# Kernel tuning notes

Measured on AMD Instinct MI355X. Metric: run time of the kernel, lower is better.

## Reference

```python
import jax, jax.numpy as jnp
import numpy as np

CH = 256
HEADS = 4
RED = 8  # SE reduction on 2*CH channels


def _conv2d(x, w, pad):
    # x: [b,c,h,w], w: [o,i,kh,kw]
    return jax.lax.conv_general_dilated(
        x, w, window_strides=(1, 1), padding=[(pad, pad), (pad, pad)],
        dimension_numbers=('NCHW', 'OIHW', 'NCHW'))


def setup_inputs() -> dict:
    key = jax.random.key(0)
    ks = jax.random.split(key, 12)
    b, c, h, w = 4, CH, 64, 64
    c2 = 2 * c
    s = 0.02
    inp = {
        'color_feat': jax.random.normal(ks[0], (b, c, h, w), jnp.float32),
        'gray_feat': jax.random.normal(ks[1], (b, c, h, w), jnp.float32),
        'Wq': jax.random.normal(ks[2], (c, c), jnp.float32) * s,
        'Wk': jax.random.normal(ks[3], (c, c), jnp.float32) * s,
        'Wv': jax.random.normal(ks[4], (c, c), jnp.float32) * s,
        'Wproj': jax.random.normal(ks[5], (c, c), jnp.float32) * s,
        'ca_w1': jax.random.normal(ks[6], (c2 // RED, c2), jnp.float32) * s,
        'ca_w2': jax.random.normal(ks[7], (c2, c2 // RED), jnp.float32) * s,
        'sa_w': jax.random.normal(ks[8], (1, 2, 7, 7), jnp.float32) * s,
        'fuse_w': jax.random.normal(ks[9], (c, c2, 3, 3), jnp.float32) * s,
        'bn_gamma': jnp.ones((c,), jnp.float32),
        'bn_beta': jnp.zeros((c,), jnp.float32),
        'bn_mean': jnp.zeros((c,), jnp.float32),
        'bn_var': jnp.ones((c,), jnp.float32),
    }
    return inp


def reference(color_feat, gray_feat, Wq, Wk, Wv, Wproj, ca_w1, ca_w2,
              sa_w, fuse_w, bn_gamma, bn_beta, bn_mean, bn_var):
    b, c, h, w = color_feat.shape
    nh = HEADS
    d = c // nh
    scale = d ** -0.5

    def heads(x, W):
        # 1x1 conv then split heads: [b,c,h,w] -> [b,nh,hw,d]
        y = jnp.einsum('bchw,oc->bohw', x, W)
        return y.reshape(b, nh, d, h * w).transpose(0, 1, 3, 2)

    q = heads(color_feat, Wq)
    k = heads(gray_feat, Wk)
    v = heads(gray_feat, Wv)

    attn = jax.nn.softmax(jnp.einsum('bnid,bnjd->bnij', q, k) * scale, axis=-1)
    out = jnp.einsum('bnij,bnjd->bnid', attn, v)
    out = out.transpose(0, 1, 3, 2).reshape(b, c, h, w)
    out = jnp.einsum('bchw,oc->bohw', out, Wproj)

    cat = jnp.concatenate([out, gray_feat], axis=1)  # [b,2c,h,w]

    # Channel attention (SE with shared MLP on avg- and max-pooled vectors)
    def mlp(z):
        return jax.nn.relu(z @ ca_w1.T) @ ca_w2.T
    avg = cat.mean(axis=(2, 3))
    mx = cat.max(axis=(2, 3))
    wch = jax.nn.sigmoid(mlp(avg) + mlp(mx))[:, :, None, None]
    cat = cat * wch

    # Spatial attention: channel-mean/max -> 7x7 conv -> sigmoid gate
    sa_in = jnp.stack([cat.mean(axis=1), cat.max(axis=1)], axis=1)  # [b,2,h,w]
    wsp = jax.nn.sigmoid(_conv2d(sa_in, sa_w, pad=3))
    cat = cat * wsp

    # Fuse: 3x3 conv -> BatchNorm (inference stats) -> LeakyReLU(0.2)
    y = _conv2d(cat, fuse_w, pad=1)
    inv = bn_gamma / jnp.sqrt(bn_var + 1e-5)
    y = (y - bn_mean[None, :, None, None]) * inv[None, :, None, None] + bn_beta[None, :, None, None]
    return jnp.where(y > 0, y, 0.2 * y)
```

## Files before the change

### kernel.cpp

```cpp
#include <hip/hip_runtime.h>
#include <hip/hip_bf16.h>
#include <stdint.h>

#define HW_ 4096

typedef short bf16x8 __attribute__((ext_vector_type(8)));
typedef short short4v __attribute__((ext_vector_type(4)));
typedef short short8v __attribute__((ext_vector_type(8)));
typedef float f32x4 __attribute__((ext_vector_type(4)));
typedef float f32x16 __attribute__((ext_vector_type(16)));
typedef uint32_t u32x4 __attribute__((ext_vector_type(4)));

__device__ inline unsigned short f2bf(float x) {
  uint32_t u = __builtin_bit_cast(uint32_t, x);
  uint32_t r = ((u >> 16) & 1u) + 0x7fffu;
  return (unsigned short)((u + r) >> 16);
}
__device__ inline uint32_t cvt_pk_bf16(float lo, float hi) {
  uint32_t r;
  asm("v_cvt_pk_bf16_f32 %0, %1, %2" : "=v"(r) : "v"(lo), "v"(hi));
  return r;
}
__device__ inline float bf_lo(uint32_t u) { return __builtin_bit_cast(float, u << 16); }
__device__ inline float bf_hi(uint32_t u) { return __builtin_bit_cast(float, u & 0xffff0000u); }
__device__ inline void gld_lds16(const unsigned short* g, unsigned short* l) {
  __builtin_amdgcn_global_load_lds((const __attribute__((address_space(1))) void*)g,
                                   (__attribute__((address_space(3))) void*)l, 16, 0, 0);
}

#define WAIT_BARRIER(VMSTR)                                                  \
  asm volatile("s_waitcnt " VMSTR "\n\ts_barrier" ::: "memory");             \
  __builtin_amdgcn_sched_barrier(0);

__global__ __launch_bounds__(256) void xconv_kernel(
    const float* __restrict__ X, unsigned short* __restrict__ Y) {
  const int i = blockIdx.x * 256 + threadIdx.x;
  const int p = i & 4095;
  const int cg = (i >> 12) & 31;
  const int b = i >> 17;
  const float* src = X + ((size_t)b * 256 + cg * 8) * HW_ + p;
  float v[8];
#pragma unroll
  for (int e = 0; e < 8; ++e) v[e] = src[(size_t)e * HW_];
  uint4 o;
  o.x = cvt_pk_bf16(v[0], v[1]);
  o.y = cvt_pk_bf16(v[2], v[3]);
  o.z = cvt_pk_bf16(v[4], v[5]);
  o.w = cvt_pk_bf16(v[6], v[7]);
  *(uint4*)&Y[((size_t)(b * 32 + cg) * HW_ + p) * 8] = o;
}

__global__ __launch_bounds__(256) void prep_kernel(
    const float* __restrict__ Wq, const float* __restrict__ Wk,
    const float* __restrict__ Wv, const float* __restrict__ Wp,
    const float* __restrict__ fw,
    unsigned short* __restrict__ WqB, unsigned short* __restrict__ WkB,
    unsigned short* __restrict__ WvB, unsigned short* __restrict__ WpB,
    unsigned short* __restrict__ wt) {
  const int blk = blockIdx.x;
  if (blk < 128) {
    const int which = blk >> 5;
    const float* W = which == 0 ? Wq : which == 1 ? Wk : which == 2 ? Wv : Wp;
    unsigned short* Y = which == 0 ? WqB : which == 1 ? WkB : which == 2 ? WvB : WpB;
    const int i = (blk & 31) * 256 + threadIdx.x;
    const int o = i & 255;
    const int cg = i >> 8;
    float4 a = *(const float4*)&W[(size_t)o * 256 + cg * 8];
    float4 bq = *(const float4*)&W[(size_t)o * 256 + cg * 8 + 4];
    uint4 ov;
    ov.x = cvt_pk_bf16(a.x, a.y);
    ov.y = cvt_pk_bf16(a.z, a.w);
    ov.z = cvt_pk_bf16(bq.x, bq.y);
    ov.w = cvt_pk_bf16(bq.z, bq.w);
    *(uint4*)&Y[((size_t)cg * 256 + o) * 8] = ov;
  } else {
    const size_t i = (size_t)(blk - 128) * 256 + threadIdx.x;
    const int oc = (int)(i >> 9);
    const int ic = (int)(i & 511);
    const float* src = fw + i * 9;
#pragma unroll
    for (int tap = 0; tap < 9; ++tap)
      wt[((size_t)tap * 256 + oc) * 512 + ic] = f2bf(src[tap]);
  }
}

#define GSTAGE(KS, BUF)                                                       \
  gld_lds16(Xb + ((size_t)((KS) * 2 + (t >> 7)) * HW_ + p0 + (t & 127)) * 8,  \
            &X_l[BUF][0][0][0] + (size_t)t * 8);
#define GCOMP(KS)                                                             \
  {                                                                           \
    bf16x8 af = *(const bf16x8*)&W_l[(KS) * 2 + g32][wo * 32 + n][0];         \
    bf16x8 b0 = *(const bf16x8*)&X_l[(KS) & 3][g32][wp * 64 + n][0];          \
    bf16x8 b1 = *(const bf16x8*)&X_l[(KS) & 3][g32][wp * 64 + 32 + n][0];     \
    acc[0] = __builtin_amdgcn_mfma_f32_32x32x16_bf16(af, b0, acc[0], 0, 0, 0);\
    acc[1] = __builtin_amdgcn_mfma_f32_32x32x16_bf16(af, b1, acc[1], 0, 0, 0);\
  }

__global__ __launch_bounds__(256) void gemm_mfma_kernel(
    const unsigned short* __restrict__ Xbf, const unsigned short* __restrict__ Wbf,
    void* __restrict__ Yv, int mode, float oscale) {
  __shared__ unsigned short W_l[32][64][8];
  __shared__ unsigned short X_l[4][2][128][8];
  const int t = threadIdx.x;
  const int w = t >> 6;
  const int l = t & 63;
  const int n = l & 31;
  const int g32 = l >> 5;
  const int p0 = blockIdx.x * 128;
  const int o0 = blockIdx.y * 64;
  const int b = blockIdx.z;
  const int wo = w >> 1, wp = w & 1;
  const unsigned short* Xb = Xbf + (size_t)b * 32 * HW_ * 8;

#pragma unroll
  for (int j = 0; j < 8; ++j) {
    const int i = j * 256 + t;
    gld_lds16(Wbf + ((size_t)(i >> 6) * 256 + o0 + (i & 63)) * 8,
              &W_l[0][0][0] + (size_t)i * 8);
  }
  GSTAGE(0, 0)
  GSTAGE(1, 1)
  GSTAGE(2, 2)

  f32x16 acc[2] = {};
  for (int ks = 0; ks < 13; ++ks) {
    WAIT_BARRIER("vmcnt(2)")
    GSTAGE(ks + 3, (ks + 3) & 3)
    GCOMP(ks)
  }
  WAIT_BARRIER("vmcnt(2)")
  GCOMP(13)
  WAIT_BARRIER("vmcnt(1)")
  GCOMP(14)
  WAIT_BARRIER("vmcnt(0)")
  GCOMP(15)

  if (mode == 1) {
    unsigned short* Y = (unsigned short*)Yv;
    const size_t bh = (size_t)b * 4 + blockIdx.y;
#pragma unroll
    for (int pf = 0; pf < 2; ++pf) {
      const int p = p0 + wp * 64 + pf * 32 + n;
      unsigned short* dst = Y + (bh * HW_ + p) * 64 + wo * 32 + 4 * g32;
#pragma unroll
      for (int q = 0; q < 4; ++q) {
        uint2 uu;
        uu.x = cvt_pk_bf16(acc[pf][q * 4 + 0] * oscale, acc[pf][q * 4 + 1] * oscale);
        uu.y = cvt_pk_bf16(acc[pf][q * 4 + 2] * oscale, acc[pf][q * 4 + 3] * oscale);
        *(uint2*)&dst[8 * q] = uu;
      }
    }
  } else if (mode == 2) {
    unsigned short* Y = (unsigned short*)Yv;
#pragma unroll
    for (int pf = 0; pf < 2; ++pf) {
      const int p = p0 + wp * 64 + pf * 32 + n;
#pragma unroll
      for (int r = 0; r < 16; ++r) {
        const int m = (r & 3) + 8 * (r >> 2) + 4 * g32;
        Y[((size_t)b * 256 + o0 + wo * 32 + m) * HW_ + p] = f2bf(acc[pf][r]);
      }
    }
  } else {
    unsigned short* Y = (unsigned short*)Yv;
    const int cgb = (o0 + wo * 32) >> 3;
#pragma unroll
    for (int pf = 0; pf < 2; ++pf) {
      const int p = p0 + wp * 64 + pf * 32 + n;
#pragma unroll
      for (int q = 0; q < 4; ++q) {
        uint2 uu;
        uu.x = cvt_pk_bf16(acc[pf][q * 4 + 0], acc[pf][q * 4 + 1]);
        uu.y = cvt_pk_bf16(acc[pf][q * 4 + 2], acc[pf][q * 4 + 3]);
        *(uint2*)&Y[((size_t)(b * 32 + cgb + q) * HW_ + p) * 8 + 4 * g32] = uu;
      }
    }
  }
}

#define ATTN_STAGE(SB)                                                       \
  {                                                                          \
    gld_lds16(gKp, kst + (SB) * 4096);                                       \
    gld_lds16(gKp + 8 * 64, kst + (SB) * 4096 + 512);                        \
    gld_lds16(gVp, vst + (SB) * 4096);                                       \
    gld_lds16(gVp + (size_t)8 * HW_, vst + (SB) * 4096 + 512);               \
    gKp += 4096;                                                             \
    gVp += 64;                                                               \
  }

#define ATTN_COMPUTE(BUF)                                                    \
  {                                                                          \
    f32x16 aS0 = zero16, aS1 = zero16;                                       \
    _Pragma("unroll") for (int s = 0; s < 4; ++s) {                          \
      bf16x8 kf0 = *(const bf16x8*)&k_l[(BUF) * 4096 + rowKA + kox[s]];      \
      bf16x8 kf1 = *(const bf16x8*)&k_l[(BUF) * 4096 + rowKB + kox[s]];      \
      aS0 = __builtin_amdgcn_mfma_f32_32x32x16_bf16(kf0, qf[s], aS0, 0, 0, 0); \
      aS1 = __builtin_amdgcn_mfma_f32_32x32x16_bf16(kf1, qf[s], aS1, 0, 0, 0); \
    }                                                                        \
    float ex0[16], ex1[16];                                                  \
    float rs = 0.f;                                                          \
    _Pragma("unroll") for (int r = 0; r < 16; ++r) {                         \
      ex0[r] = __builtin_amdgcn_exp2f(aS0[r]);                               \
      ex1[r] = __builtin_amdgcn_exp2f(aS1[r]);                               \
      rs += ex0[r] + ex1[r];                                                 \
    }                                                                        \
    l_r += rs;                                                               \
    union { u32x4 u4; bf16x8 v8; } pA, pB, pC, pD;                           \
    pA.u4 = (u32x4){cvt_pk_bf16(ex0[0], ex0[1]), cvt_pk_bf16(ex0[2], ex0[3]),    \
                    cvt_pk_bf16(ex0[4], ex0[5]), cvt_pk_bf16(ex0[6], ex0[7])};   \
    pB.u4 = (u32x4){cvt_pk_bf16(ex0[8], ex0[9]), cvt_pk_bf16(ex0[10], ex0[11]),  \
                    cvt_pk_bf16(ex0[12], ex0[13]), cvt_pk_bf16(ex0[14], ex0[15])};\
    pC.u4 = (u32x4){cvt_pk_bf16(ex1[0], ex1[1]), cvt_pk_bf16(ex1[2], ex1[3]),    \
                    cvt_pk_bf16(ex1[4], ex1[5]), cvt_pk_bf16(ex1[6], ex1[7])};   \
    pD.u4 = (u32x4){cvt_pk_bf16(ex1[8], ex1[9]), cvt_pk_bf16(ex1[10], ex1[11]),  \
                    cvt_pk_bf16(ex1[12], ex1[13]), cvt_pk_bf16(ex1[14], ex1[15])};\
    _Pragma("unroll") for (int dh = 0; dh < 2; ++dh) {                       \
      const int rw = (BUF) * 4096 + (dh * 32 + n) * 64;                      \
      union { short4v h2[2]; bf16x8 v8; } v0, v1, v2, v3;                    \
      v0.h2[0] = *(const short4v*)&v_l[rw + voA0];                           \
      v0.h2[1] = *(const short4v*)&v_l[rw + voA1];                           \
      v1.h2[0] = *(const short4v*)&v_l[rw + voB0];                           \
      v1.h2[1] = *(const short4v*)&v_l[rw + voB1];                           \
      v2.h2[0] = *(const short4v*)&v_l[rw + voC0];                           \
      v2.h2[1] = *(const short4v*)&v_l[rw + voC1];                           \
      v3.h2[0] = *(const short4v*)&v_l[rw + voD0];                           \
      v3.h2[1] = *(const short4v*)&v_l[rw + voD1];                           \
      f32x16 ac = accO[dh];                                                  \
      ac = __builtin_amdgcn_mfma_f32_32x32x16_bf16(v0.v8, pA.v8, ac, 0, 0, 0); \
      ac = __builtin_amdgcn_mfma_f32_32x32x16_bf16(v1.v8, pB.v8, ac, 0, 0, 0); \
      ac = __builtin_amdgcn_mfma_f32_32x32x16_bf16(v2.v8, pC.v8, ac, 0, 0, 0); \
      ac = __builtin_amdgcn_mfma_f32_32x32x16_bf16(v3.v8, pD.v8, ac, 0, 0, 0); \
      accO[dh] = ac;                                                         \
    }                                                                        \
  }

#define ATTN_PHASE(B, SB, VMSTR, DOST)                                       \
  WAIT_BARRIER(VMSTR)                                                        \
  if (DOST) { ATTN_STAGE(SB) }                                               \
  ATTN_COMPUTE(B)

__global__ __launch_bounds__(256) void attn_mfma_kernel(
    const unsigned short* __restrict__ Qb, const unsigned short* __restrict__ Kb,
    const unsigned short* __restrict__ Vb, unsigned short* __restrict__ Abf) {
  __shared__ unsigned short k_l[4 * 4096];
  __shared__ unsigned short v_l[4 * 4096];
  const int t = threadIdx.x;
  const int w = t >> 6;
  const int l = t & 63;
  const int n = l & 31;
  const int h = l >> 5;
  const int bid = blockIdx.x;
  const int gidx = (bid & 7) * 64 + (bid >> 3);
  const int bn = gidx >> 5;
  const int q0 = (gidx & 31) * 128 + w * 32;

  bf16x8 qf[4];
#pragma unroll
  for (int s = 0; s < 4; ++s)
    qf[s] = *(const bf16x8*)&Qb[((size_t)bn * HW_ + q0 + n) * 64 + s * 16 + h * 8];

  const int n7 = n & 7;
  const int rowKA = n * 64;
  const int rowKB = (32 + n) * 64;
  int kox[4];
#pragma unroll
  for (int s = 0; s < 4; ++s) kox[s] = ((2 * s + h) ^ n7) * 8;
  const int h4 = 4 * h;
  const int voA0 = ((0 ^ n7) * 8) + h4, voA1 = ((1 ^ n7) * 8) + h4;
  const int voB0 = ((2 ^ n7) * 8) + h4, voB1 = ((3 ^ n7) * 8) + h4;
  const int voC0 = ((4 ^ n7) * 8) + h4, voC1 = ((5 ^ n7) * 8) + h4;
  const int voD0 = ((6 ^ n7) * 8) + h4, voD1 = ((7 ^ n7) * 8) + h4;

  const int srow = 16 * w + (l >> 3);
  const int schunk = (l & 7) ^ ((l >> 3) & 7);
  const unsigned short* gKp = Kb + ((size_t)bn * HW_ + srow) * 64 + schunk * 8;
  const unsigned short* gVp = Vb + ((size_t)bn * 64 + srow) * HW_ + schunk * 8;
  unsigned short* kst = k_l + w * 1024;
  unsigned short* vst = v_l + w * 1024;

  f32x16 accO[2] = {};
  float l_r = 0.f;
  const f32x16 zero16 = {};

  ATTN_STAGE(0)
  ATTN_STAGE(1)

  for (int t4 = 0; t4 < 15; ++t4) {
    ATTN_PHASE(0, 2, "vmcnt(4)", 1)
    ATTN_PHASE(1, 3, "vmcnt(4)", 1)
    ATTN_PHASE(2, 0, "vmcnt(4)", 1)
    ATTN_PHASE(3, 1, "vmcnt(4)", 1)
  }
  ATTN_PHASE(0, 2, "vmcnt(4)", 1)
  ATTN_PHASE(1, 3, "vmcnt(4)", 1)
  ATTN_PHASE(2, 0, "vmcnt(4)", 0)
  ATTN_PHASE(3, 0, "vmcnt(0)", 0)

  const int head = bn & 3;
  const int bb = bn >> 2;
  const float lsum = l_r + __shfl_xor(l_r, 32);
  const float inv = 1.0f / lsum;
  const int pcol = q0 + n;
#pragma unroll
  for (int dh = 0; dh < 2; ++dh)
#pragma unroll
    for (int k4 = 0; k4 < 4; ++k4) {
      uint2 uu;
      uu.x = cvt_pk_bf16(accO[dh][k4 * 4 + 0] * inv, accO[dh][k4 * 4 + 1] * inv);
      uu.y = cvt_pk_bf16(accO[dh][k4 * 4 + 2] * inv, accO[dh][k4 * 4 + 3] * inv);
      const int cg = head * 8 + dh * 4 + k4;
      *(uint2*)&Abf[((size_t)(bb * 32 + cg) * HW_ + pcol) * 8 + h4] = uu;
    }
}

__global__ __launch_bounds__(256) void pool_kernel(
    const unsigned short* __restrict__ Pbf, const unsigned short* __restrict__ Gbf,
    float* __restrict__ psum, float* __restrict__ pmaxH) {
  const int cg = blockIdx.x;
  const int b = blockIdx.y;
  const int half = blockIdx.z;
  const int t = threadIdx.x;
  const unsigned short* P = Pbf + ((size_t)(b * 32 + cg) * HW_ + half * 2048) * 8;
  const unsigned short* G = Gbf + ((size_t)(b * 32 + cg) * HW_ + half * 2048) * 8;
  float s[16], m[16];
#pragma unroll
  for (int i = 0; i < 16; ++i) { s[i] = 0.f; m[i] = -1e30f; }
  for (int p = t; p < 2048; p += 256) {
    uint4 a = *(const uint4*)&P[(size_t)p * 8];
    uint4 gg = *(const uint4*)&G[(size_t)p * 8];
    const uint32_t ua[4] = {a.x, a.y, a.z, a.w};
    const uint32_t ug[4] = {gg.x, gg.y, gg.z, gg.w};
#pragma unroll
    for (int q = 0; q < 4; ++q) {
      const float a0 = bf_lo(ua[q]), a1 = bf_hi(ua[q]);
      const float g0 = bf_lo(ug[q]), g1 = bf_hi(ug[q]);
      s[q * 2] += a0; s[q * 2 + 1] += a1;
      m[q * 2] = fmaxf(m[q * 2], a0); m[q * 2 + 1] = fmaxf(m[q * 2 + 1], a1);
      s[8 + q * 2] += g0; s[8 + q * 2 + 1] += g1;
      m[8 + q * 2] = fmaxf(m[8 + q * 2], g0); m[8 + q * 2 + 1] = fmaxf(m[8 + q * 2 + 1], g1);
    }
  }
#pragma unroll
  for (int i = 0; i < 16; ++i)
#pragma unroll
    for (int off = 1; off < 64; off <<= 1) {
      s[i] += __shfl_xor(s[i], off);
      m[i] = fmaxf(m[i], __shfl_xor(m[i], off));
    }
  __shared__ float red[4][32];
  const int wv = t >> 6;
  if ((t & 63) == 0) {
#pragma unroll
    for (int i = 0; i < 16; ++i) { red[wv][i] = s[i]; red[wv][16 + i] = m[i]; }
  }
  __syncthreads();
  if (t < 32) {
    const float v0 = red[0][t], v1 = red[1][t], v2 = red[2][t], v3 = red[3][t];
    if (t < 16) {
      const int ch = (t < 8) ? cg * 8 + t : 256 + cg * 8 + (t - 8);
      psum[half * 2048 + b * 512 + ch] = v0 + v1 + v2 + v3;
    } else {
      const int i = t - 16;
      const int ch = (i < 8) ? cg * 8 + i : 256 + cg * 8 + (i - 8);
      pmaxH[half * 2048 + b * 512 + ch] = fmaxf(fmaxf(v0, v1), fmaxf(v2, v3));
    }
  }
}

__global__ __launch_bounds__(256) void se_kernel(
    const float* __restrict__ psum, const float* __restrict__ pmaxH,
    const float* __restrict__ w1, const float* __restrict__ w2,
    float* __restrict__ wch) {
  const int b = blockIdx.x;
  const int t = threadIdx.x;
  __shared__ float za[512], zm[512], hs[64];
  za[t] = (psum[b * 512 + t] + psum[2048 + b * 512 + t]) * (1.f / 4096.f);
  za[256 + t] = (psum[b * 512 + 256 + t] + psum[2048 + b * 512 + 256 + t]) * (1.f / 4096.f);
  zm[t] = fmaxf(pmaxH[b * 512 + t], pmaxH[2048 + b * 512 + t]);
  zm[256 + t] = fmaxf(pmaxH[b * 512 + 256 + t], pmaxH[2048 + b * 512 + 256 + t]);
  __syncthreads();
  if (t < 64) {
    float ha = 0.f, hm = 0.f;
    for (int c = 0; c < 512; ++c) {
      const float w = w1[t * 512 + c];
      ha += w * za[c];
      hm += w * zm[c];
    }
    hs[t] = fmaxf(ha, 0.f) + fmaxf(hm, 0.f);
  }
  __syncthreads();
  for (int o = t; o < 512; o += 256) {
    float acc = 0.f;
#pragma unroll
    for (int hh = 0; hh < 64; ++hh) acc += hs[hh] * w2[o * 64 + hh];
    wch[b * 512 + o] = 1.f / (1.f + __expf(-acc));
  }
}

__global__ __launch_bounds__(256) void sa_reduce_kernel(
    const unsigned short* __restrict__ Pbf, const unsigned short* __restrict__ Gbf,
    const float* __restrict__ wch, float* __restrict__ sa_in) {
  const int b = blockIdx.y;
  const int t = threadIdx.x;
  const int px = t & 63;
  const int sl = t >> 6;
  const int p = blockIdx.x * 64 + px;
  __shared__ float wl[512];
  __shared__ float sred[4][64], mred[4][64];
  wl[t] = wch[b * 512 + t];
  wl[256 + t] = wch[b * 512 + 256 + t];
  __syncthreads();
  float s = 0.f, mx = -1e30f;
#pragma unroll 4
  for (int k = 0; k < 16; ++k) {
    const int chunk = sl * 16 + k;
    const unsigned short* src = (chunk < 32)
        ? &Pbf[((size_t)(b * 32 + chunk) * HW_ + p) * 8]
        : &Gbf[((size_t)(b * 32 + (chunk - 32)) * HW_ + p) * 8];
    uint4 a = *(const uint4*)src;
    const uint32_t u[4] = {a.x, a.y, a.z, a.w};
#pragma unroll
    for (int q = 0; q < 4; ++q) {
      const float v0 = bf_lo(u[q]) * wl[chunk * 8 + q * 2];
      const float v1 = bf_hi(u[q]) * wl[chunk * 8 + q * 2 + 1];
      s += v0 + v1;
      mx = fmaxf(mx, fmaxf(v0, v1));
    }
  }
  sred[sl][px] = s;
  mred[sl][px] = mx;
  __syncthreads();
  if (sl == 0) {
    const float S = sred[0][px] + sred[1][px] + sred[2][px] + sred[3][px];
    const float M = fmaxf(fmaxf(mred[0][px], mred[1][px]), fmaxf(mred[2][px], mred[3][px]));
    sa_in[((size_t)b * 2 + 0) * HW_ + p] = S * (1.f / 512.f);
    sa_in[((size_t)b * 2 + 1) * HW_ + p] = M;
  }
}

__global__ __launch_bounds__(256) void sa_conv_kernel(
    const float* __restrict__ sa_in, const float* __restrict__ sa_w,
    float* __restrict__ wsp) {
  const int b = blockIdx.y;
  const int t = threadIdx.x;
  __shared__ float pl[2][64][64];
  __shared__ float wl[98];
  for (int e = t; e < 8192; e += 256) ((float*)pl)[e] = sa_in[(size_t)b * 8192 + e];
  if (t < 98) wl[t] = sa_w[t];
  __syncthreads();
  const int pix = blockIdx.x * 256 + t;
  const int y = pix >> 6, x = pix & 63;
  float acc = 0.f;
#pragma unroll
  for (int ic = 0; ic < 2; ++ic)
#pragma unroll
    for (int ky = 0; ky < 7; ++ky) {
      const int yy = y + ky - 3;
      if (yy < 0 || yy > 63) continue;
#pragma unroll
      for (int kx = 0; kx < 7; ++kx) {
        const int xx = x + kx - 3;
        if (xx < 0 || xx > 63) continue;
        acc += pl[ic][yy][xx] * wl[ic * 49 + ky * 7 + kx];
      }
    }
  wsp[(size_t)b * HW_ + pix] = 1.f / (1.f + __expf(-acc));
}

__global__ __launch_bounds__(256) void gate_kernel(
    const unsigned short* __restrict__ Pbf, const unsigned short* __restrict__ Gbf,
    const float* __restrict__ wch, const float* __restrict__ wsp,
    unsigned short* __restrict__ catg) {
  const int yp = blockIdx.x;
  const int b = blockIdx.y;
  const int t = threadIdx.x;
  unsigned short* rowp = catg + ((size_t)b * 66 + yp) * 80 * 512;
  if (yp == 0 || yp == 65) {
    short8v z = {};
    for (int m = t; m < 5120; m += 256) *(short8v*)&rowp[m * 8] = z;
    return;
  }
  const int y = yp - 1;
  __shared__ unsigned short tile[64][512];
  __shared__ float wchl[512];
  __shared__ float wspl[64];
  for (int e = t; e < 512; e += 256) wchl[e] = wch[b * 512 + e];
  if (t < 64) wspl[t] = wsp[(size_t)b * HW_ + y * 64 + t];
  {
    short8v z = {};
    for (int m = t; m < 1024; m += 256) {
      const int col = m >> 6;
      const int xi = (col < 8) ? col : (col + 64);
      *(short8v*)&rowp[(size_t)xi * 512 + (m & 63) * 8] = z;
    }
  }
  __syncthreads();
  const int x = t & 63;
  const int cs = t >> 6;
  const float wx = wspl[x];
#pragma unroll
  for (int k = 0; k < 16; ++k) {
    const int chunk = cs * 16 + k;
    const unsigned short* src = (chunk < 32)
        ? &Pbf[((size_t)(b * 32 + chunk) * HW_ + y * 64 + x) * 8]
        : &Gbf[((size_t)(b * 32 + (chunk - 32)) * HW_ + y * 64 + x) * 8];
    uint4 a = *(const uint4*)src;
    const uint32_t u[4] = {a.x, a.y, a.z, a.w};
    uint32_t o[4];
#pragma unroll
    for (int q = 0; q < 4; ++q) {
      const float lo = bf_lo(u[q]) * wchl[chunk * 8 + q * 2] * wx;
      const float hi = bf_hi(u[q]) * wchl[chunk * 8 + q * 2 + 1] * wx;
      o[q] = cvt_pk_bf16(lo, hi);
    }
    uint4 ov = {o[0], o[1], o[2], o[3]};
    *(uint4*)&tile[x][(chunk ^ (x & 7)) * 8] = ov;
  }
  __syncthreads();
#pragma unroll
  for (int j = 0; j < 16; ++j) {
    const int xi = (t >> 6) + 4 * j;
    const int c8 = t & 63;
    uint4 v = *(const uint4*)&tile[xi][(c8 ^ (xi & 7)) * 8];
    *(uint4*)&rowp[(size_t)(xi + 8) * 512 + c8 * 8] = v;
  }
}

__global__ __launch_bounds__(256) void fuse_mfma_kernel(
    const unsigned short* __restrict__ catg, const unsigned short* __restrict__ wt,
    const float* __restrict__ bn_g, const float* __restrict__ bn_b,
    const float* __restrict__ bn_m, const float* __restrict__ bn_v,
    float* __restrict__ out) {
  __shared__ unsigned short X_l[2][6][2][80][8];
  __shared__ unsigned short W_l[2][9][2][32][8];
  __shared__ float invl[32], shl[32];
  const int t = threadIdx.x;
  const int w = t >> 6;
  const int l = t & 63;
  const int n = l & 31;
  const int g = l >> 5;
  const int i = blockIdx.x;
  const int xcd = i & 7, slot = i >> 3;
  const int ocB = slot & 7;
  const int yb = xcd + 8 * (slot >> 3);
  const int y0 = (yb & 15) * 4;
  const int o0 = ocB * 32;
  const int b = yb >> 4;

  if (t < 32) {
    const float iv = bn_g[o0 + t] * rsqrtf(bn_v[o0 + t] + 1e-5f);
    invl[t] = iv;
    shl[t] = bn_b[o0 + t] - bn_m[o0 + t] * iv;
  }

  const unsigned short* catb = catg + ((size_t)b * 66 + y0) * 80 * 512;

  auto stageX = [&](int bi, int ic0) {
    for (int wc = w; wc < 15; wc += 4) {
      const int m = wc * 64 + l;
      const int lr = m / 160;
      const int rem = m - lr * 160;
      const int half = rem / 80;
      const int xi = rem - half * 80;
      gld_lds16(catb + ((size_t)lr * 80 + xi) * 512 + ic0 + half * 8,
                &X_l[bi][0][0][0][0] + (size_t)wc * 512);
    }
  };
  auto stageW = [&](int bi, int ic0) {
    for (int wc = w; wc < 9; wc += 4) {
      const int m = wc * 64 + l;
      const int tap = m >> 6;
      const int rem = m & 63;
      const int half = rem >> 5;
      const int oc = rem & 31;
      gld_lds16(wt + ((size_t)tap * 256 + o0 + oc) * 512 + ic0 + half * 8,
                &W_l[bi][0][0][0][0] + (size_t)wc * 512);
    }
  };

  f32x16 acc[2] = {};

  stageX(0, 0);
  stageW(0, 0);
  int buf = 0;
  for (int ks = 0; ks < 32; ++ks) {
    asm volatile("s_waitcnt vmcnt(0)" ::: "memory");
    __syncthreads();
    if (ks < 31) {
      stageX(buf ^ 1, (ks + 1) * 16);
      stageW(buf ^ 1, (ks + 1) * 16);
    }
#pragma unroll
    for (int ky = 0; ky < 3; ++ky) {
      const int lr = w + ky;
#pragma unroll
      for (int kx = 0; kx < 3; ++kx) {
        const int tap = ky * 3 + kx;
        bf16x8 a0 = *(const bf16x8*)&W_l[buf][tap][g][n][0];
        bf16x8 b0 = *(const bf16x8*)&X_l[buf][lr][g][n + kx + 7][0];
        bf16x8 b1 = *(const bf16x8*)&X_l[buf][lr][g][32 + n + kx + 7][0];
        acc[0] = __builtin_amdgcn_mfma_f32_32x32x16_bf16(a0, b0, acc[0], 0, 0, 0);
        acc[1] = __builtin_amdgcn_mfma_f32_32x32x16_bf16(a0, b1, acc[1], 0, 0, 0);
      }
    }
    buf ^= 1;
  }

#pragma unroll
  for (int pf = 0; pf < 2; ++pf)
#pragma unroll
    for (int r = 0; r < 16; ++r) {
      const int row = (r & 3) + 8 * (r >> 2) + 4 * g;
      const float yv = acc[pf][r] * invl[row] + shl[row];
      const float ov = yv > 0.f ? yv : 0.2f * yv;
      out[((size_t)b * 256 + o0 + row) * HW_ + (size_t)(y0 + w) * 64 + pf * 32 + n] = ov;
    }
}

extern "C" void kernel_launch(void* const* d_in, const int* in_sizes, int n_in,
                              void* d_out, int out_size, void* d_ws, size_t ws_size,
                              hipStream_t stream) {
  const float* color  = (const float*)d_in[0];
  const float* gray   = (const float*)d_in[1];
  const float* Wq     = (const float*)d_in[2];
  const float* Wk     = (const float*)d_in[3];
  const float* Wv     = (const float*)d_in[4];
  const float* Wproj  = (const float*)d_in[5];
  const float* ca_w1  = (const float*)d_in[6];
  const float* ca_w2  = (const float*)d_in[7];
  const float* sa_w   = (const float*)d_in[8];
  const float* fuse_w = (const float*)d_in[9];
  const float* bn_g   = (const float*)d_in[10];
  const float* bn_b   = (const float*)d_in[11];
  const float* bn_m   = (const float*)d_in[12];
  const float* bn_v   = (const float*)d_in[13];
  float* out = (float*)d_out;

  char* ws = (char*)d_ws;
  unsigned short* Cbf = (unsigned short*)(ws);
  unsigned short* Gbf = (unsigned short*)(ws + (8u << 20));
  unsigned short* Qbf = (unsigned short*)(ws + (16u << 20));
  unsigned short* Kbf = (unsigned short*)(ws + (24u << 20));
  unsigned short* Vbf = (unsigned short*)(ws + (32u << 20));
  unsigned short* Abf = (unsigned short*)(ws);
  unsigned short* Pbf = (unsigned short*)(ws + (16u << 20));
  unsigned short* catg = (unsigned short*)(ws + (24u << 20));
  unsigned short* WqB = (unsigned short*)(ws + (45u << 20));
  unsigned short* WkB = WqB + 65536;
  unsigned short* WvB = WkB + 65536;
  unsigned short* WpB = WvB + 65536;
  unsigned short* Wt  = (unsigned short*)(ws + (45u << 20) + (1u << 19));
  float* psum  = (float*)(ws + (48u << 20));
  float* pmaxH = psum + 4096;
  float* wch   = pmaxH + 4096;
  float* sa_in = wch + 2048;
  float* wsp   = sa_in + 32768;
  (void)in_sizes; (void)n_in; (void)out_size; (void)ws_size;

  const float qscale = 0.125f * 1.44269504f;

  prep_kernel<<<dim3(640), 256, 0, stream>>>(Wq, Wk, Wv, Wproj, fuse_w,
                                             WqB, WkB, WvB, WpB, Wt);
  xconv_kernel<<<dim3(2048), 256, 0, stream>>>(color, Cbf);
  xconv_kernel<<<dim3(2048), 256, 0, stream>>>(gray, Gbf);

  dim3 g_gemm(32, 4, 4);
  gemm_mfma_kernel<<<g_gemm, 256, 0, stream>>>(Cbf, WqB, Qbf, 1, qscale);
  gemm_mfma_kernel<<<g_gemm, 256, 0, stream>>>(Gbf, WkB, Kbf, 1, 1.0f);
  gemm_mfma_kernel<<<g_gemm, 256, 0, stream>>>(Gbf, WvB, Vbf, 2, 1.0f);
  attn_mfma_kernel<<<dim3(512), 256, 0, stream>>>(Qbf, Kbf, Vbf, Abf);
  gemm_mfma_kernel<<<g_gemm, 256, 0, stream>>>(Abf, WpB, Pbf, 3, 1.0f);

  pool_kernel<<<dim3(32, 4, 2), 256, 0, stream>>>(Pbf, Gbf, psum, pmaxH);
  se_kernel<<<dim3(4), 256, 0, stream>>>(psum, pmaxH, ca_w1, ca_w2, wch);
  sa_reduce_kernel<<<dim3(64, 4), 256, 0, stream>>>(Pbf, Gbf, wch, sa_in);
  sa_conv_kernel<<<dim3(16, 4), 256, 0, stream>>>(sa_in, sa_w, wsp);
  gate_kernel<<<dim3(66, 4), 256, 0, stream>>>(Pbf, Gbf, wch, wsp, catg);
  fuse_mfma_kernel<<<dim3(512), 256, 0, stream>>>(catg, Wt, bn_g, bn_b, bn_m, bn_v, out);
}
```

Baseline: 260.9 us.

## Fuse K/V projections, add MFMA priority hints, split gate kernel across x-halves

The K and V 1x1-conv GEMMs now run in one kernel that stages the shared gray-feature tile once and drives both weight matrices, which removes a launch and a second read of the input. s_setprio raises wave priority around the MFMA sections in the attention and fuse kernels. The softmax row-sum is split into four partial accumulators to shorten the dependency chain. The gate kernel grid gains a dimension that splits each row in half, giving more blocks and a smaller LDS tile. The fused GEMM holds twice the accumulators, which raises register pressure.

```diff
diff --git a/kernel.cpp b/kernel.cpp
--- a/kernel.cpp
+++ b/kernel.cpp
@@ -150,17 +150,6 @@
         *(uint2*)&dst[8 * q] = uu;
       }
     }
-  } else if (mode == 2) {
-    unsigned short* Y = (unsigned short*)Yv;
-#pragma unroll
-    for (int pf = 0; pf < 2; ++pf) {
-      const int p = p0 + wp * 64 + pf * 32 + n;
-#pragma unroll
-      for (int r = 0; r < 16; ++r) {
-        const int m = (r & 3) + 8 * (r >> 2) + 4 * g32;
-        Y[((size_t)b * 256 + o0 + wo * 32 + m) * HW_ + p] = f2bf(acc[pf][r]);
-      }
-    }
   } else {
     unsigned short* Y = (unsigned short*)Yv;
     const int cgb = (o0 + wo * 32) >> 3;
@@ -174,6 +163,85 @@
         uu.y = cvt_pk_bf16(acc[pf][q * 4 + 2], acc[pf][q * 4 + 3]);
         *(uint2*)&Y[((size_t)(b * 32 + cgb + q) * HW_ + p) * 8 + 4 * g32] = uu;
       }
+    }
+  }
+}
+
+#define GCOMP_KV(KS)                                                          \
+  {                                                                           \
+    bf16x8 afk = *(const bf16x8*)&W_l[0][(KS) * 2 + g32][wo * 32 + n][0];     \
+    bf16x8 afv = *(const bf16x8*)&W_l[1][(KS) * 2 + g32][wo * 32 + n][0];     \
+    bf16x8 b0 = *(const bf16x8*)&X_l[(KS) & 3][g32][wp * 64 + n][0];          \
+    bf16x8 b1 = *(const bf16x8*)&X_l[(KS) & 3][g32][wp * 64 + 32 + n][0];     \
+    accK[0] = __builtin_amdgcn_mfma_f32_32x32x16_bf16(afk, b0, accK[0], 0, 0, 0); \
+    accK[1] = __builtin_amdgcn_mfma_f32_32x32x16_bf16(afk, b1, accK[1], 0, 0, 0); \
+    accV[0] = __builtin_amdgcn_mfma_f32_32x32x16_bf16(afv, b0, accV[0], 0, 0, 0); \
+    accV[1] = __builtin_amdgcn_mfma_f32_32x32x16_bf16(afv, b1, accV[1], 0, 0, 0); \
+  }
+
+__global__ __launch_bounds__(256) void gemm_kv_kernel(
+    const unsigned short* __restrict__ Xbf, const unsigned short* __restrict__ WkB,
+    const unsigned short* __restrict__ WvB, unsigned short* __restrict__ Kout,
+    unsigned short* __restrict__ Vout) {
+  __shared__ unsigned short W_l[2][32][64][8];
+  __shared__ unsigned short X_l[4][2][128][8];
+  const int t = threadIdx.x;
+  const int w = t >> 6;
+  const int l = t & 63;
+  const int n = l & 31;
+  const int g32 = l >> 5;
+  const int p0 = blockIdx.x * 128;
+  const int o0 = blockIdx.y * 64;
+  const int b = blockIdx.z;
+  const int wo = w >> 1, wp = w & 1;
+  const unsigned short* Xb = Xbf + (size_t)b * 32 * HW_ * 8;
+
+#pragma unroll
+  for (int j = 0; j < 16; ++j) {
+    const int i = j * 256 + t;
+    const int ii = i & 2047;
+    const unsigned short* Wsrc = (i >> 11) ? WvB : WkB;
+    gld_lds16(Wsrc + ((size_t)(ii >> 6) * 256 + o0 + (ii & 63)) * 8,
+              &W_l[0][0][0][0] + (size_t)i * 8);
+  }
+  GSTAGE(0, 0)
+  GSTAGE(1, 1)
+  GSTAGE(2, 2)
+
+  f32x16 accK[2] = {};
+  f32x16 accV[2] = {};
+  for (int ks = 0; ks < 13; ++ks) {
+    WAIT_BARRIER("vmcnt(2)")
+    GSTAGE(ks + 3, (ks + 3) & 3)
+    GCOMP_KV(ks)
+  }
+  WAIT_BARRIER("vmcnt(2)")
+  GCOMP_KV(13)
+  WAIT_BARRIER("vmcnt(1)")
+  GCOMP_KV(14)
+  WAIT_BARRIER("vmcnt(0)")
+  GCOMP_KV(15)
+
+  const size_t bh = (size_t)b * 4 + blockIdx.y;
+#pragma unroll
+  for (int pf = 0; pf < 2; ++pf) {
+    const int p = p0 + wp * 64 + pf * 32 + n;
+    unsigned short* dst = Kout + (bh * HW_ + p) * 64 + wo * 32 + 4 * g32;
+#pragma unroll
+    for (int q = 0; q < 4; ++q) {
+      uint2 uu;
+      uu.x = cvt_pk_bf16(accK[pf][q * 4 + 0], accK[pf][q * 4 + 1]);
+      uu.y = cvt_pk_bf16(accK[pf][q * 4 + 2], accK[pf][q * 4 + 3]);
+      *(uint2*)&dst[8 * q] = uu;
+    }
+  }
+#pragma unroll
+  for (int pf = 0; pf < 2; ++pf) {
+    const int p = p0 + wp * 64 + pf * 32 + n;
+#pragma unroll
+    for (int r = 0; r < 16; ++r) {
+      const int m = (r & 3) + 8 * (r >> 2) + 4 * g32;
+      Vout[((size_t)b * 256 + o0 + wo * 32 + m) * HW_ + p] = f2bf(accV[pf][r]);
     }
   }
 }
@@ -191,20 +259,27 @@
 #define ATTN_COMPUTE(BUF)                                                    \
   {                                                                          \
     f32x16 aS0 = zero16, aS1 = zero16;                                       \
+    __builtin_amdgcn_s_setprio(1);                                           \
     _Pragma("unroll") for (int s = 0; s < 4; ++s) {                          \
       bf16x8 kf0 = *(const bf16x8*)&k_l[(BUF) * 4096 + rowKA + kox[s]];      \
       bf16x8 kf1 = *(const bf16x8*)&k_l[(BUF) * 4096 + rowKB + kox[s]];      \
       aS0 = __builtin_amdgcn_mfma_f32_32x32x16_bf16(kf0, qf[s], aS0, 0, 0, 0); \
       aS1 = __builtin_amdgcn_mfma_f32_32x32x16_bf16(kf1, qf[s], aS1, 0, 0, 0); \
     }                                                                        \
+    __builtin_amdgcn_s_setprio(0);                                           \
     float ex0[16], ex1[16];                                                  \
-    float rs = 0.f;                                                          \
     _Pragma("unroll") for (int r = 0; r < 16; ++r) {                         \
       ex0[r] = __builtin_amdgcn_exp2f(aS0[r]);                               \
       ex1[r] = __builtin_amdgcn_exp2f(aS1[r]);                               \
-      rs += ex0[r] + ex1[r];                                                 \
     }                                                                        \
-    l_r += rs;                                                               \
+    float rsp0 = 0.f, rsp1 = 0.f, rsp2 = 0.f, rsp3 = 0.f;                    \
+    _Pragma("unroll") for (int r = 0; r < 16; r += 4) {                      \
+      rsp0 += ex0[r + 0] + ex1[r + 0];                                       \
+      rsp1 += ex0[r + 1] + ex1[r + 1];                                       \
+      rsp2 += ex0[r + 2] + ex1[r + 2];                                       \
+      rsp3 += ex0[r + 3] + ex1[r + 3];                                       \
+    }                                                                        \
+    l_r += (rsp0 + rsp1) + (rsp2 + rsp3);                                    \
     union { u32x4 u4; bf16x8 v8; } pA, pB, pC, pD;                           \
     pA.u4 = (u32x4){cvt_pk_bf16(ex0[0], ex0[1]), cvt_pk_bf16(ex0[2], ex0[3]),    \
                     cvt_pk_bf16(ex0[4], ex0[5]), cvt_pk_bf16(ex0[6], ex0[7])};   \
@@ -214,6 +289,7 @@
                     cvt_pk_bf16(ex1[4], ex1[5]), cvt_pk_bf16(ex1[6], ex1[7])};   \
     pD.u4 = (u32x4){cvt_pk_bf16(ex1[8], ex1[9]), cvt_pk_bf16(ex1[10], ex1[11]),  \
                     cvt_pk_bf16(ex1[12], ex1[13]), cvt_pk_bf16(ex1[14], ex1[15])};\
+    __builtin_amdgcn_s_setprio(1);                                           \
     _Pragma("unroll") for (int dh = 0; dh < 2; ++dh) {                       \
       const int rw = (BUF) * 4096 + (dh * 32 + n) * 64;                      \
       union { short4v h2[2]; bf16x8 v8; } v0, v1, v2, v3;                    \
@@ -232,6 +308,7 @@
       ac = __builtin_amdgcn_mfma_f32_32x32x16_bf16(v3.v8, pD.v8, ac, 0, 0, 0); \
       accO[dh] = ac;                                                         \
     }                                                                        \
+    __builtin_amdgcn_s_setprio(0);                                           \
   }
 
 #define ATTN_PHASE(B, SB, VMSTR, DOST)                                       \
@@ -472,35 +549,36 @@
     const float* __restrict__ wch, const float* __restrict__ wsp,
     unsigned short* __restrict__ catg) {
   const int yp = blockIdx.x;
-  const int b = blockIdx.y;
+  const int xh = blockIdx.y;
+  const int b = blockIdx.z;
   const int t = threadIdx.x;
   unsigned short* rowp = catg + ((size_t)b * 66 + yp) * 80 * 512;
   if (yp == 0 || yp == 65) {
     short8v z = {};
-    for (int m = t; m < 5120; m += 256) *(short8v*)&rowp[m * 8] = z;
+    for (int m = t; m < 2560; m += 256)
+      *(short8v*)&rowp[((size_t)xh * 40 * 512) + m * 8] = z;
     return;
   }
   const int y = yp - 1;
-  __shared__ unsigned short tile[64][512];
+  __shared__ unsigned short tile[32][512];
   __shared__ float wchl[512];
-  __shared__ float wspl[64];
+  __shared__ float wspl[32];
   for (int e = t; e < 512; e += 256) wchl[e] = wch[b * 512 + e];
-  if (t < 64) wspl[t] = wsp[(size_t)b * HW_ + y * 64 + t];
+  if (t < 32) wspl[t] = wsp[(size_t)b * HW_ + y * 64 + xh * 32 + t];
   {
     short8v z = {};
-    for (int m = t; m < 1024; m += 256) {
-      const int col = m >> 6;
-      const int xi = (col < 8) ? col : (col + 64);
-      *(short8v*)&rowp[(size_t)xi * 512 + (m & 63) * 8] = z;
-    }
+    const int xbase = xh ? 72 : 0;
+    for (int m = t; m < 512; m += 256)
+      *(short8v*)&rowp[(size_t)(xbase + (m >> 6)) * 512 + (m & 63) * 8] = z;
   }
   __syncthreads();
-  const int x = t & 63;
-  const int cs = t >> 6;
-  const float wx = wspl[x];
-#pragma unroll
-  for (int k = 0; k < 16; ++k) {
-    const int chunk = cs * 16 + k;
+  const int xl = t & 31;
+  const int x = xh * 32 + xl;
+  const int cs = t >> 5;
+  const float wx = wspl[xl];
+#pragma unroll
+  for (int k = 0; k < 8; ++k) {
+    const int chunk = cs * 8 + k;
     const unsigned short* src = (chunk < 32)
         ? &Pbf[((size_t)(b * 32 + chunk) * HW_ + y * 64 + x) * 8]
         : &Gbf[((size_t)(b * 32 + (chunk - 32)) * HW_ + y * 64 + x) * 8];
@@ -514,15 +592,16 @@
       o[q] = cvt_pk_bf16(lo, hi);
     }
     uint4 ov = {o[0], o[1], o[2], o[3]};
-    *(uint4*)&tile[x][(chunk ^ (x & 7)) * 8] = ov;
+    *(uint4*)&tile[xl][(chunk ^ (xl & 7)) * 8] = ov;
   }
   __syncthreads();
 #pragma unroll
-  for (int j = 0; j < 16; ++j) {
-    const int xi = (t >> 6) + 4 * j;
-    const int c8 = t & 63;
-    uint4 v = *(const uint4*)&tile[xi][(c8 ^ (xi & 7)) * 8];
-    *(uint4*)&rowp[(size_t)(xi + 8) * 512 + c8 * 8] = v;
+  for (int j = 0; j < 8; ++j) {
+    const int idx = j * 256 + t;
+    const int xi_l = idx >> 6;
+    const int c8 = idx & 63;
+    uint4 v = *(const uint4*)&tile[xi_l][(c8 ^ (xi_l & 7)) * 8];
+    *(uint4*)&rowp[(size_t)(xh * 32 + xi_l + 8) * 512 + c8 * 8] = v;
   }
 }
 
@@ -590,6 +669,7 @@
       stageX(buf ^ 1, (ks + 1) * 16);
       stageW(buf ^ 1, (ks + 1) * 16);
     }
+    __builtin_amdgcn_s_setprio(1);
 #pragma unroll
     for (int ky = 0; ky < 3; ++ky) {
       const int lr = w + ky;
@@ -603,6 +683,7 @@
         acc[1] = __builtin_amdgcn_mfma_f32_32x32x16_bf16(a0, b1, acc[1], 0, 0, 0);
       }
     }
+    __builtin_amdgcn_s_setprio(0);
     buf ^= 1;
   }
 
@@ -666,8 +747,7 @@
 
   dim3 g_gemm(32, 4, 4);
   gemm_mfma_kernel<<<g_gemm, 256, 0, stream>>>(Cbf, WqB, Qbf, 1, qscale);
-  gemm_mfma_kernel<<<g_gemm, 256, 0, stream>>>(Gbf, WkB, Kbf, 1, 1.0f);
-  gemm_mfma_kernel<<<g_gemm, 256, 0, stream>>>(Gbf, WvB, Vbf, 2, 1.0f);
+  gemm_kv_kernel<<<g_gemm, 256, 0, stream>>>(Gbf, WkB, WvB, Kbf, Vbf);
   attn_mfma_kernel<<<dim3(512), 256, 0, stream>>>(Qbf, Kbf, Vbf, Abf);
   gemm_mfma_kernel<<<g_gemm, 256, 0, stream>>>(Abf, WpB, Pbf, 3, 1.0f);
 
@@ -675,6 +755,6 @@
   se_kernel<<<dim3(4), 256, 0, stream>>>(psum, pmaxH, ca_w1, ca_w2, wch);
   sa_reduce_kernel<<<dim3(64, 4), 256, 0, stream>>>(Pbf, Gbf, wch, sa_in);
   sa_conv_kernel<<<dim3(16, 4), 256, 0, stream>>>(sa_in, sa_w, wsp);
-  gate_kernel<<<dim3(66, 4), 256, 0, stream>>>(Pbf, Gbf, wch, wsp, catg);
+  gate_kernel<<<dim3(66, 2, 4), 256, 0, stream>>>(Pbf, Gbf, wch, wsp, catg);
   fuse_mfma_kernel<<<dim3(512), 256, 0, stream>>>(catg, Wt, bn_g, bn_b, bn_m, bn_v, out);
 }
```

Measured after the change: 252.9 us. 1.03x faster.
